# Kernel optimization log

Measured on AMD Instinct MI355X. Metric: run time of the kernel, lower is better.

The kernel has to match this reference:

```python
import jax, jax.numpy as jnp
import numpy as np
from jax.scipy.special import logsumexp

B, S, T = 256, 1024, 73  # batch, seq_len, num_tags (1 + 2*36 BIO labels)
N_SLOTS = 36


def _build_type_indices():
    # Reproduce CRF.build_transitions index construction from label strings.
    vocab = ['O'] + [f'{p}-slot{i}' for i in range(N_SLOTS) for p in ('B', 'I')]
    m1 = {'O': 0, 'B': 1, 'I': 2}
    m2 = {'O': 0, 'B': 3, 'I': 4}
    t0 = np.zeros((T, T), np.int32)
    t1 = np.zeros((T, T), np.int32)
    for i, li in enumerate(vocab):
        for j, lj in enumerate(vocab):
            if li != 'O' and li[2:] != lj[2:]:
                t0[i, j] = m1[li[0]]; t1[i, j] = m2[lj[0]]
            else:
                t0[i, j] = m1[li[0]]; t1[i, j] = m1[lj[0]]
    return t0, t1


def setup_inputs() -> dict:
    key = jax.random.key(0)
    k1, k2, k3, k4 = jax.random.split(key, 4)
    feats = jax.random.normal(k1, (B, S, T), dtype=jnp.float32)
    mask = jnp.ones((B, S), dtype=bool)
    tags = jax.random.randint(k2, (B, S), 0, T)
    cdt_transitions = jnp.log(jnp.array(
        [[0.6, 0.4, 0.001, 0.001, 0.001],
         [0.3, 0.1, 0.1, 0.5, 0.001],
         [0.6, 0.1, 0.1, 0.2, 0.001]], dtype=jnp.float32))
    start_transitions = jax.random.normal(k3, (T,), dtype=jnp.float32)
    stop_transitions = jax.random.normal(k4, (T,), dtype=jnp.float32)
    t0, t1 = _build_type_indices()
    return {
        'feats': feats, 'mask': mask, 'tags': tags,
        'cdt_transitions': cdt_transitions,
        'start_transitions': start_transitions,
        'stop_transitions': stop_transitions,
        'types0': jnp.asarray(t0), 'types1': jnp.asarray(t1),
    }


def reference(feats, mask, tags, cdt_transitions, start_transitions,
              stop_transitions, types0, types1):
    # compute_loss = forward_alg(partition) - score_sentence(gold)
    trans = cdt_transitions[types0, types1]  # [T, T]
    maskf = mask.astype(feats.dtype)

    # ---- forward algorithm (log partition) via scan over time ----
    part0 = feats[:, 0] + start_transitions[None]  # [B, T]

    def step(partition, inp):
        f_t, m_t = inp  # [B, T], [B]
        # cur_values[b, i, j] = f_t[b, j] + partition[b, i] + trans[i, j]
        cur = f_t[:, None, :] + partition[:, :, None] + trans[None]
        cp = logsumexp(cur, axis=1)  # [B, T]
        return jnp.where(m_t[:, None], cp, partition), None

    feats_t = jnp.swapaxes(feats, 0, 1)  # [S, B, T]
    mask_t = jnp.swapaxes(mask, 0, 1)    # [S, B]
    partition, _ = jax.lax.scan(step, part0, (feats_t[1:], mask_t[1:]))
    forward_score = logsumexp(partition + stop_transitions[None], axis=1)  # [B]

    # ---- gold score ----
    feat_score = (jnp.take_along_axis(feats, tags[..., None], axis=2)[..., 0]
                  * maskf).sum(-1)
    trans_score = (trans[tags[:, :-1], tags[:, 1:]] * maskf[:, 1:]).sum(-1)
    lengths = mask.sum(1).astype(jnp.int32)  # [B]
    end_ids = jnp.take_along_axis(tags, (lengths - 1)[:, None], axis=1)[:, 0]
    gold_score = (feat_score + start_transitions[tags[:, 0]]
                  + trans_score + stop_transitions[end_ids])

    return forward_score - gold_score  # [B] per-sentence NLL
```

## Files before the change

### kernel.cpp

```cpp
#include <hip/hip_runtime.h>
#include <hip/hip_bf16.h>
#include <math.h>

#define T_TAGS 73
#define SEQ    1024
#define NBATCH 256

__device__ __forceinline__ float rl_f(float v, int lane) {
  return __int_as_float(__builtin_amdgcn_readlane(__float_as_int(v), lane));
}
template<int N>
__device__ __forceinline__ float dpp_ror_add(float v) {
  int s = __builtin_amdgcn_update_dpp(0, __float_as_int(v), 0x120 + N, 0xF, 0xF, false);
  return v + __int_as_float(s);
}
__device__ __forceinline__ float rowsum16(float v) {
  v = dpp_ror_add<8>(v); v = dpp_ror_add<4>(v);
  v = dpp_ror_add<2>(v); v = dpp_ror_add<1>(v);
  return v;
}

template<bool BWD>
__device__ __forceinline__ void scan_half(
    const float* __restrict__ fbase, int t0,
    int off1, int off2, float mB, float mI, bool isO,
    float c1B, float c2B, float c3B,
    float c1I, float c2I, float c3I,
    float c1O, float c2O, float c3O,
    float a11, float a12, float a21, float a22,
    float& wB, float& wI, float& acc)
{
  const float L2E = 1.4426950408889634f;
  const int DT   = BWD ? -1 : 1;
  const int NBLK = 31;
  const int TAIL = BWD ? 16 : 15;

  auto idx = [&](int i) { return (size_t)(t0 + DT * i) * T_TAGS; };

  auto step = [&](float eB, float eI, bool renorm) {
    float xB = BWD ? wB * eB : wB;
    float xI = BWD ? wI * eI : wI;
    float xO = rl_f(xB, 48);
    float sB = rowsum16(xB);
    float sI = rowsum16(xI);
    float SB = (rl_f(sB, 0) + rl_f(sB, 16)) + rl_f(sB, 32);
    float SI = (rl_f(sI, 0) + rl_f(sI, 16)) + rl_f(sI, 32);
    float KB = fmaf(SI, c3B, fmaf(SB, c2B, xO * c1B));
    float KI = fmaf(SI, c3I, fmaf(SB, c2I, xO * c1I));
    float KO = fmaf(SI, c3O, fmaf(SB, c2O, xO * c1O));
    float vB = fmaf(xB, a11, fmaf(xI, a12, KB));
    float vI = fmaf(xB, a21, fmaf(xI, a22, KI));
    vB = isO ? KO : vB;
    if (renorm) {
      float T = (SB + SI) + xO;
      float r = __builtin_amdgcn_rcpf(T);
      acc += __builtin_amdgcn_logf(T);
      if (BWD) { wB = vB * r;        wI = vI * r;        }
      else     { wB = vB * (eB * r); wI = vI * (eI * r); }
    } else {
      if (BWD) { wB = vB;            wI = vI;            }
      else     { wB = vB * eB;       wI = vI * eI;       }
    }
  };

  float efB[16], efI[16], rfB[16], rfI[16];
  #pragma unroll
  for (int k = 0; k < 16; ++k) {
    rfB[k] = fbase[idx(k) + off1];
    rfI[k] = fbase[idx(k) + off2];
  }
  #pragma unroll
  for (int k = 0; k < 16; ++k) {
    efB[k] = mB * __builtin_amdgcn_exp2f(rfB[k] * L2E);
    efI[k] = mI * __builtin_amdgcn_exp2f(rfI[k] * L2E);
    rfB[k] = fbase[idx(16 + k) + off1];
    rfI[k] = fbase[idx(16 + k) + off2];
  }
  for (int m = 0; m < NBLK; ++m) {
    #pragma unroll
    for (int k = 0; k < 16; ++k) {
      step(efB[k], efI[k], (k & 7) == 7);
      efB[k] = mB * __builtin_amdgcn_exp2f(rfB[k] * L2E);
      efI[k] = mI * __builtin_amdgcn_exp2f(rfI[k] * L2E);
      size_t a = idx(16 * m + k + 32);
      rfB[k] = fbase[a + off1];
      rfI[k] = fbase[a + off2];
    }
  }
  #pragma unroll
  for (int k = 0; k < 16; ++k)
    if (k < TAIL) step(efB[k], efI[k], (k & 7) == 7);
}

extern "C" __global__ void __launch_bounds__(192, 1)
crf_fused_kernel(const float* __restrict__ feats, const int* __restrict__ tags,
                 const float* __restrict__ cdt, const float* __restrict__ start_t,
                 const float* __restrict__ stop_t, float* __restrict__ out)
{
  __shared__ float s_cdt[15];
  __shared__ float s_wB[37], s_wI[37], s_vB[37], s_vI[37];
  __shared__ float s_acc[2];
  __shared__ float s_gold;

  const int tid = threadIdx.x;
  const int b   = blockIdx.x;
  const float* fbase = feats + (size_t)b * (SEQ * T_TAGS);

  if (tid < 15) s_cdt[tid] = cdt[tid];
  __syncthreads();

  const float L2E = 1.4426950408889634f;
  const float LN2 = 0.69314718055994531f;

  if (tid < 128) {
    const int  s      = tid & 63;
    const bool isBwd  = (tid >= 64);
    const bool isSlot = (s < 36);
    const bool isO    = (s == 48);
    const int  off1   = isSlot ? (1 + 2 * s) : 0;
    const int  off2   = isSlot ? (2 + 2 * s) : 0;
    const float mB    = (isSlot || isO) ? 1.f : 0.f;
    const float mI    = isSlot ? 1.f : 0.f;

    #define EXPC(i) __builtin_amdgcn_exp2f(cdt[i] * L2E)
    const float E00 = EXPC(0),  E01 = EXPC(1),  E02 = EXPC(2);
    const float E10 = EXPC(5),  E11 = EXPC(6),  E12 = EXPC(7),  E13 = EXPC(8),  E14 = EXPC(9);
    const float E20 = EXPC(10), E21 = EXPC(11), E22 = EXPC(12), E23 = EXPC(13), E24 = EXPC(14);
    #undef EXPC
    const float dBB = E11 - E13, dIB = E21 - E23;
    const float dBI = E12 - E14, dII = E22 - E24;

    float wB, wI, acc = 0.f;
    if (!isBwd) {
      wB = mB * __builtin_amdgcn_exp2f((fbase[off1] + start_t[off1]) * L2E);
      wI = mI * __builtin_amdgcn_exp2f((fbase[off2] + start_t[off2]) * L2E);
      scan_half<false>(fbase, 1, off1, off2, mB, mI, isO,
                       E01, E13, E23,   E02, E14, E24,   E00, E10, E20,
                       dBB, dIB, dBI, dII, wB, wI, acc);
      if (isSlot) { s_wB[s] = wB; s_wI[s] = wI; }
      if (isO)    { s_wB[36] = wB; s_wI[36] = 0.f; }
      if (s == 0) s_acc[0] = acc;
    } else {
      wB = mB * __builtin_amdgcn_exp2f(stop_t[off1] * L2E);
      wI = mI * __builtin_amdgcn_exp2f(stop_t[off2] * L2E);
      scan_half<true>(fbase, SEQ - 1, off1, off2, mB, mI, isO,
                      E10, E13, E14,   E20, E23, E24,   E00, E01, E02,
                      dBB, dBI, dIB, dII, wB, wI, acc);
      if (isSlot) { s_vB[s] = wB; s_vI[s] = wI; }
      if (isO)    { s_vB[36] = wB; s_vI[36] = 0.f; }
      if (s == 0) s_acc[1] = acc;
    }
  } else {
    const int L = tid - 128;
    const int* tg = tags + (size_t)b * SEQ;
    float acc = 0.f;
    #pragma unroll 4
    for (int k = 0; k < 16; ++k) {
      int t   = L + 64 * k;
      int tag = tg[t];
      acc += fbase[t * T_TAGS + tag];
      if (t < SEQ - 1) {
        int tag2 = tg[t + 1];
        int  a     = (tag == 0) ? 0 : ((tag & 1) ? 1 : 2);
        bool useM1 = (tag == 0) ||
                     ((tag2 != 0) && (((tag - 1) >> 1) == ((tag2 - 1) >> 1)));
        int  c = (tag2 == 0) ? 0
                             : (useM1 ? ((tag2 & 1) ? 1 : 2)
                                      : ((tag2 & 1) ? 3 : 4));
        acc += s_cdt[a * 5 + c];
      }
      if (t == 0)       acc += start_t[tag];
      if (t == SEQ - 1) acc += stop_t[tag];
    }
    float g = rowsum16(acc);
    float gold = (rl_f(g, 0) + rl_f(g, 16)) + (rl_f(g, 32) + rl_f(g, 48));
    if (tid == 128) s_gold = gold;
  }

  __syncthreads();

  if (tid < 64) {
    const int s = tid;
    float p = 0.f;
    if (s < 37) p = s_wB[s] * s_vB[s] + s_wI[s] * s_vI[s];
    float e = rowsum16(p);
    float S = (rl_f(e, 0) + rl_f(e, 16)) + rl_f(e, 32);
    float fwd = LN2 * ((s_acc[0] + s_acc[1]) + __builtin_amdgcn_logf(S));
    if (tid == 0) out[b] = fwd - s_gold;
  }
}

extern "C" void kernel_launch(void* const* d_in, const int* in_sizes, int n_in,
                              void* d_out, int out_size, void* d_ws, size_t ws_size,
                              hipStream_t stream) {
  const float* feats   = (const float*)d_in[0];
  const int*   tags    = (const int*)d_in[2];
  const float* cdt     = (const float*)d_in[3];
  const float* start_t = (const float*)d_in[4];
  const float* stop_t  = (const float*)d_in[5];
  float* out = (float*)d_out;

  crf_fused_kernel<<<dim3(NBATCH), dim3(192), 0, stream>>>(
      feats, tags, cdt, start_t, stop_t, out);
}
```

Baseline: 62.35 us.

## Stage feature loads through LDS with async global_load_lds ring buffer

Replaces the register-prefetched global loads in the forward/backward scan with asynchronous global-to-LDS loads into a 4-slot ring buffer, three groups of 8 timesteps ahead, synchronized via explicit vmcnt waits. The goal is to cut register pressure and hide global memory latency behind the serial recurrence. In exchange it uses 32KB of shared memory, adds LDS reads on the critical path, and depends on correct vmcnt accounting for the wait counts.

Result: slower. 69.71 us (+11.8%).

```diff
diff --git a/kernel.cpp b/kernel.cpp
--- a/kernel.cpp
+++ b/kernel.cpp
@@ -20,9 +20,19 @@
   return v;
 }
 
+__device__ __forceinline__ void load1_lds(const float* g, float* l) {
+  __builtin_amdgcn_global_load_lds(
+      (const __attribute__((address_space(1))) void*)g,
+      (__attribute__((address_space(3))) void*)l, 4, 0, 0);
+}
+template<int N>
+__device__ __forceinline__ void waitv() {
+  asm volatile("s_waitcnt vmcnt(%0)" :: "n"(N) : "memory");
+}
+
 template<bool BWD>
-__device__ __forceinline__ void scan_half(
-    const float* __restrict__ fbase, int t0,
+__device__ __forceinline__ void scan_stage(
+    const float* __restrict__ fbase, float* stage, int lane,
     int off1, int off2, float mB, float mI, bool isO,
     float c1B, float c2B, float c3B,
     float c1I, float c2I, float c3I,
@@ -31,18 +41,26 @@
     float& wB, float& wI, float& acc)
 {
   const float L2E = 1.4426950408889634f;
-  const int DT   = BWD ? -1 : 1;
-  const int NBLK = 31;
-  const int TAIL = BWD ? 16 : 15;
-
-  auto idx = [&](int i) { return (size_t)(t0 + DT * i) * T_TAGS; };
+  const int NG = 64;
+
+  auto gaddr = [&](int g, int k) {
+    int t = BWD ? (1023 - 8 * g - k) : (1 + 8 * g + k);
+    return (size_t)t * T_TAGS;
+  };
+  auto stage_group = [&](int g) {
+    float* base = stage + (g & 3) * 1024;
+    #pragma unroll
+    for (int k = 0; k < 8; ++k) {
+      load1_lds(fbase + gaddr(g, k) + off1, base + k * 128);
+      load1_lds(fbase + gaddr(g, k) + off2, base + k * 128 + 64);
+    }
+  };
 
   auto step = [&](float eB, float eI, bool renorm) {
     float xB = BWD ? wB * eB : wB;
     float xI = BWD ? wI * eI : wI;
     float xO = rl_f(xB, 48);
-    float sB = rowsum16(xB);
-    float sI = rowsum16(xI);
+    float sB = rowsum16(xB), sI = rowsum16(xI);
     float SB = (rl_f(sB, 0) + rl_f(sB, 16)) + rl_f(sB, 32);
     float SI = (rl_f(sI, 0) + rl_f(sI, 16)) + rl_f(sI, 32);
     float KB = fmaf(SI, c3B, fmaf(SB, c2B, xO * c1B));
@@ -63,33 +81,29 @@
     }
   };
 
-  float efB[16], efI[16], rfB[16], rfI[16];
-  #pragma unroll
-  for (int k = 0; k < 16; ++k) {
-    rfB[k] = fbase[idx(k) + off1];
-    rfI[k] = fbase[idx(k) + off2];
+  auto consume = [&](int g, int cnt) {
+    const float* base = stage + (g & 3) * 1024;
+    float efB[8], efI[8];
+    #pragma unroll
+    for (int k = 0; k < 8; ++k)
+      if (k < cnt) {
+        efB[k] = mB * __builtin_amdgcn_exp2f(base[k * 128 + lane] * L2E);
+        efI[k] = mI * __builtin_amdgcn_exp2f(base[k * 128 + 64 + lane] * L2E);
+      }
+    #pragma unroll
+    for (int k = 0; k < 8; ++k)
+      if (k < cnt) step(efB[k], efI[k], k == 7);
+  };
+
+  stage_group(0); stage_group(1); stage_group(2);
+  for (int g = 0; g < NG - 3; ++g) {
+    waitv<32>();
+    consume(g, 8);
+    stage_group(g + 3);
   }
-  #pragma unroll
-  for (int k = 0; k < 16; ++k) {
-    efB[k] = mB * __builtin_amdgcn_exp2f(rfB[k] * L2E);
-    efI[k] = mI * __builtin_amdgcn_exp2f(rfI[k] * L2E);
-    rfB[k] = fbase[idx(16 + k) + off1];
-    rfI[k] = fbase[idx(16 + k) + off2];
-  }
-  for (int m = 0; m < NBLK; ++m) {
-    #pragma unroll
-    for (int k = 0; k < 16; ++k) {
-      step(efB[k], efI[k], (k & 7) == 7);
-      efB[k] = mB * __builtin_amdgcn_exp2f(rfB[k] * L2E);
-      efI[k] = mI * __builtin_amdgcn_exp2f(rfI[k] * L2E);
-      size_t a = idx(16 * m + k + 32);
-      rfB[k] = fbase[a + off1];
-      rfI[k] = fbase[a + off2];
-    }
-  }
-  #pragma unroll
-  for (int k = 0; k < 16; ++k)
-    if (k < TAIL) step(efB[k], efI[k], (k & 7) == 7);
+  waitv<32>(); consume(NG - 3, 8);
+  waitv<16>(); consume(NG - 2, 8);
+  waitv<0>();  consume(NG - 1, BWD ? 7 : 8);
 }
 
 extern "C" __global__ void __launch_bounds__(192, 1)
@@ -97,6 +111,7 @@
                  const float* __restrict__ cdt, const float* __restrict__ start_t,
                  const float* __restrict__ stop_t, float* __restrict__ out)
 {
+  __shared__ float s_stage[8192];
   __shared__ float s_cdt[15];
   __shared__ float s_wB[37], s_wI[37], s_vB[37], s_vI[37];
   __shared__ float s_acc[2];
@@ -113,12 +128,12 @@
   const float LN2 = 0.69314718055994531f;
 
   if (tid < 128) {
-    const int  s      = tid & 63;
+    const int  lane   = tid & 63;
     const bool isBwd  = (tid >= 64);
-    const bool isSlot = (s < 36);
-    const bool isO    = (s == 48);
-    const int  off1   = isSlot ? (1 + 2 * s) : 0;
-    const int  off2   = isSlot ? (2 + 2 * s) : 0;
+    const bool isSlot = (lane < 36);
+    const bool isO    = (lane == 48);
+    const int  off1   = isSlot ? (1 + 2 * lane) : 0;
+    const int  off2   = isSlot ? (2 + 2 * lane) : 0;
     const float mB    = (isSlot || isO) ? 1.f : 0.f;
     const float mI    = isSlot ? 1.f : 0.f;
 
@@ -134,21 +149,21 @@
     if (!isBwd) {
       wB = mB * __builtin_amdgcn_exp2f((fbase[off1] + start_t[off1]) * L2E);
       wI = mI * __builtin_amdgcn_exp2f((fbase[off2] + start_t[off2]) * L2E);
-      scan_half<false>(fbase, 1, off1, off2, mB, mI, isO,
-                       E01, E13, E23,   E02, E14, E24,   E00, E10, E20,
-                       dBB, dIB, dBI, dII, wB, wI, acc);
-      if (isSlot) { s_wB[s] = wB; s_wI[s] = wI; }
+      scan_stage<false>(fbase, &s_stage[0], lane, off1, off2, mB, mI, isO,
+                        E01, E13, E23,   E02, E14, E24,   E00, E10, E20,
+                        dBB, dIB, dBI, dII, wB, wI, acc);
+      if (isSlot) { s_wB[lane] = wB; s_wI[lane] = wI; }
       if (isO)    { s_wB[36] = wB; s_wI[36] = 0.f; }
-      if (s == 0) s_acc[0] = acc;
+      if (lane == 0) s_acc[0] = acc;
     } else {
       wB = mB * __builtin_amdgcn_exp2f(stop_t[off1] * L2E);
       wI = mI * __builtin_amdgcn_exp2f(stop_t[off2] * L2E);
-      scan_half<true>(fbase, SEQ - 1, off1, off2, mB, mI, isO,
-                      E10, E13, E14,   E20, E23, E24,   E00, E01, E02,
-                      dBB, dBI, dIB, dII, wB, wI, acc);
-      if (isSlot) { s_vB[s] = wB; s_vI[s] = wI; }
+      scan_stage<true>(fbase, &s_stage[4096], lane, off1, off2, mB, mI, isO,
+                       E10, E13, E14,   E20, E23, E24,   E00, E01, E02,
+                       dBB, dBI, dIB, dII, wB, wI, acc);
+      if (isSlot) { s_vB[lane] = wB; s_vI[lane] = wI; }
       if (isO)    { s_vB[36] = wB; s_vI[36] = 0.f; }
-      if (s == 0) s_acc[1] = acc;
+      if (lane == 0) s_acc[1] = acc;
     }
   } else {
     const int L = tid - 128;
```
